# Kernel optimization log

Hardware: AMD Instinct MI355X
Metric: run time of the kernel (lower is better)

## Reference

```python
import jax, jax.numpy as jnp
import numpy as np

B, S, D, H, F = 4, 1024, 1024, 16, 4096
DK = D // H
NEG_INF = jnp.float32(-jnp.inf)


def rmsnorm(x, gamma):
    rms = jnp.sqrt(jnp.mean(x * x, axis=-1, keepdims=True))
    return gamma * x / rms


def masked_softmax(cor):
    # softmax over last dim; rows that are entirely -inf produce all-zero rows
    # (matches the original's NaN -> 0 masked_fill).
    m = jnp.max(cor, axis=-1, keepdims=True)
    m_safe = jnp.where(jnp.isneginf(m), 0.0, m)
    e = jnp.exp(cor - m_safe)
    denom = jnp.sum(e, axis=-1, keepdims=True)
    return e / jnp.where(denom == 0.0, 1.0, denom)


def setup_inputs() -> dict:
    key = jax.random.key(0)
    ks = jax.random.split(key, 12)
    inp = {
        'src': jax.random.normal(ks[0], (B, S, D), jnp.float32),
        'src_padding_mask': jax.random.bernoulli(ks[1], 0.1, (B, S)),
        'prev': jax.random.normal(ks[2], (H, B, S, S), jnp.float32),
        'layer_ind': 2,
        'Wq': jax.random.normal(ks[3], (H, D, DK), jnp.float32) * 0.02,
        'Wk': jax.random.normal(ks[4], (H, D, DK), jnp.float32) * 0.02,
        'Wv': jax.random.normal(ks[5], (H, D, DK), jnp.float32) * 0.02,
        'Wproj': jax.random.normal(ks[6], (D, D), jnp.float32) * 0.02,
        'gamma1': jnp.ones((D,), jnp.float32),
        'gamma2': jnp.ones((D,), jnp.float32),
        'W1': jax.random.normal(ks[7], (D, F), jnp.float32) * 0.02,
        'b1': jnp.zeros((F,), jnp.float32),
        'W2': jax.random.normal(ks[8], (F, D), jnp.float32) * 0.02,
        'b2': jnp.zeros((D,), jnp.float32),
    }
    return inp


def reference(src, src_padding_mask, prev, layer_ind, Wq, Wk, Wv, Wproj,
              gamma1, gamma2, W1, b1, W2, b2):
    ln1 = rmsnorm(src, gamma1)                              # [B,S,D]
    q = jnp.einsum('bsd,hdk->hbsk', ln1, Wq)                # [H,B,S,DK]
    k = jnp.einsum('bsd,hdk->hbsk', ln1, Wk)
    v = jnp.einsum('bsd,hdk->hbsk', ln1, Wv)
    scores = jnp.einsum('hbsk,hbtk->hbst', q, k) * (DK ** -0.5)  # [H,B,S,S]
    qmask = src_padding_mask[None, :, :, None]              # query (row) pad mask
    kvmask = src_padding_mask[None, :, None, :]             # key   (col) pad mask
    scores = jnp.where(qmask, NEG_INF, scores)
    scores = jnp.where(kvmask, NEG_INF, scores)
    raw = (scores + prev) / 2                               # RealFormer residual scores
    cor = raw / (1.0 - 0.5 ** layer_ind)
    w = masked_softmax(cor)                                 # [H,B,S,S]
    att = jnp.einsum('hbst,hbtk->bshk', w, v).reshape(B, S, H * DK)
    attention = att @ Wproj + src                           # residual
    h = jax.nn.relu(rmsnorm(attention, gamma2) @ W1 + b1)
    out = attention + (h @ W2 + b2)
    return out, raw
```

## Files before the change

kernel.cpp:

```cpp
#include <hip/hip_runtime.h>
#include <math.h>

#define Bv 4
#define Sv 1024
#define Dv 1024
#define Hv 16
#define Fv 4096
#define DKv 64

#define MASK_SENTINEL (-3.0e38f)

typedef __attribute__((ext_vector_type(8))) short short8v;
typedef __attribute__((ext_vector_type(4))) float float4v;

__device__ inline unsigned short bf16_rne(float x) {
    unsigned int u = __float_as_uint(x);
    unsigned int r = (u + 0x7FFFu + ((u >> 16) & 1u)) >> 16;
    return (unsigned short)r;
}
__device__ inline float bf16_tof(unsigned short h) {
    return __uint_as_float(((unsigned int)h) << 16);
}
__device__ inline void split2(float x, unsigned short& h, unsigned short& l) {
    unsigned short hh = bf16_rne(x);
    h = hh;
    l = bf16_rne(x - bf16_tof(hh));
}

__global__ __launch_bounds__(256) void rmsnorm_split_k(const float* __restrict__ x,
                                                       const float* __restrict__ g,
                                                       unsigned short* __restrict__ yh,
                                                       unsigned short* __restrict__ yl)
{
    const int row = blockIdx.x;
    const int tid = threadIdx.x;
    const float4* xv = reinterpret_cast<const float4*>(x) + (size_t)row * (Dv / 4);
    float4 v = xv[tid];
    float ss = v.x * v.x + v.y * v.y + v.z * v.z + v.w * v.w;
    #pragma unroll
    for (int o = 32; o > 0; o >>= 1) ss += __shfl_down(ss, o);
    __shared__ float wsum[4];
    if ((tid & 63) == 0) wsum[tid >> 6] = ss;
    __syncthreads();
    const float total = wsum[0] + wsum[1] + wsum[2] + wsum[3];
    const float rinv = rsqrtf(total * (1.0f / Dv));
    const float4 gv = reinterpret_cast<const float4*>(g)[tid];
    float o0 = v.x * gv.x * rinv, o1 = v.y * gv.y * rinv;
    float o2 = v.z * gv.z * rinv, o3 = v.w * gv.w * rinv;
    ushort4 uh, ul; unsigned short h, l;
    split2(o0, h, l); uh.x = h; ul.x = l;
    split2(o1, h, l); uh.y = h; ul.y = l;
    split2(o2, h, l); uh.z = h; ul.z = l;
    split2(o3, h, l); uh.w = h; ul.w = l;
    *(ushort4*)&yh[(size_t)row * Dv + tid * 4] = uh;
    *(ushort4*)&yl[(size_t)row * Dv + tid * 4] = ul;
}

template<bool HEADW>
__global__ __launch_bounds__(256) void tsplit_k(const float* __restrict__ W,
                                                unsigned short* __restrict__ WTh,
                                                unsigned short* __restrict__ WTl,
                                                int K, int N)
{
    __shared__ float tile[64 * 68];
    const int tid = threadIdx.x;
    const int n0 = blockIdx.x * 64, k0 = blockIdx.y * 64;
    #pragma unroll
    for (int it = 0; it < 4; ++it) {
        int slot = it * 256 + tid;
        int r = slot >> 4, c4 = (slot & 15) * 4;
        const float* src;
        if (HEADW)
            src = &W[((size_t)(n0 >> 6) * K + (k0 + r)) * 64 + c4];
        else
            src = &W[(size_t)(k0 + r) * N + n0 + c4];
        *(float4*)&tile[r * 68 + c4] = *(const float4*)src;
    }
    __syncthreads();
    #pragma unroll
    for (int it = 0; it < 4; ++it) {
        int slot = it * 256 + tid;
        int rr = slot >> 4, c4 = (slot & 15) * 4;
        ushort4 uh, ul;
        unsigned short h, l;
        split2(tile[(c4 + 0) * 68 + rr], h, l); uh.x = h; ul.x = l;
        split2(tile[(c4 + 1) * 68 + rr], h, l); uh.y = h; ul.y = l;
        split2(tile[(c4 + 2) * 68 + rr], h, l); uh.z = h; ul.z = l;
        split2(tile[(c4 + 3) * 68 + rr], h, l); uh.w = h; ul.w = l;
        size_t o = (size_t)(n0 + rr) * K + k0 + c4;
        *(ushort4*)&WTh[o] = uh;
        *(ushort4*)&WTl[o] = ul;
    }
}

#define BKP 40
#define KOFF ((size_t)8 << 20)
template<int OUTM, bool RELU, bool BIAS, bool RES>
__global__ __launch_bounds__(256) void gemm64(const unsigned short* __restrict__ Ahg,
                                              const unsigned short* __restrict__ Alg,
                                              const unsigned short* __restrict__ Bhg,
                                              const unsigned short* __restrict__ Blg,
                                              const float* __restrict__ bias,
                                              const float* __restrict__ res,
                                              float* __restrict__ C,
                                              unsigned short* __restrict__ Ch,
                                              unsigned short* __restrict__ Cl,
                                              int M, int N, int K)
{
    __shared__ unsigned short Ah[64 * BKP], Al[64 * BKP];
    __shared__ unsigned short Bh[128 * BKP], Bl[128 * BKP];
    const int tid = threadIdx.x;
    const int lane = tid & 63, wid = tid >> 6;
    const int wc = wid;
    const int l15 = lane & 15, lg = lane >> 4;
    const int bm = blockIdx.y * 64, bn = blockIdx.x * 128;

    float4v acc[4][2];
    #pragma unroll
    for (int i = 0; i < 4; ++i)
        #pragma unroll
        for (int j = 0; j < 2; ++j) acc[i][j] = (float4v)(0.0f);

    const int sr = tid >> 2, sc8 = (tid & 3) * 8;

    for (int k0 = 0; k0 < K; k0 += 32) {
        *(uint4*)&Ah[sr * BKP + sc8] = *(const uint4*)&Ahg[(size_t)(bm + sr) * K + k0 + sc8];
        *(uint4*)&Al[sr * BKP + sc8] = *(const uint4*)&Alg[(size_t)(bm + sr) * K + k0 + sc8];
        #pragma unroll
        for (int it = 0; it < 2; ++it) {
            int slot = it * 256 + tid;
            int r = slot >> 2, c8 = (slot & 3) * 8;
            *(uint4*)&Bh[r * BKP + c8] = *(const uint4*)&Bhg[(size_t)(bn + r) * K + k0 + c8];
            *(uint4*)&Bl[r * BKP + c8] = *(const uint4*)&Blg[(size_t)(bn + r) * K + k0 + c8];
        }
        __syncthreads();

        short8v fah[4], fal[4], fbh[2], fbl[2];
        const int kb = lg * 8;
        #pragma unroll
        for (int mi = 0; mi < 4; ++mi) {
            int row = mi * 16 + l15;
            fah[mi] = *(const short8v*)&Ah[row * BKP + kb];
            fal[mi] = *(const short8v*)&Al[row * BKP + kb];
        }
        #pragma unroll
        for (int ni = 0; ni < 2; ++ni) {
            int row = wc * 32 + ni * 16 + l15;
            fbh[ni] = *(const short8v*)&Bh[row * BKP + kb];
            fbl[ni] = *(const short8v*)&Bl[row * BKP + kb];
        }
        #pragma unroll
        for (int mi = 0; mi < 4; ++mi)
            #pragma unroll
            for (int ni = 0; ni < 2; ++ni) {
                float4v c = acc[mi][ni];
                c = __builtin_amdgcn_mfma_f32_16x16x32_bf16(fah[mi], fbh[ni], c, 0, 0, 0);
                c = __builtin_amdgcn_mfma_f32_16x16x32_bf16(fah[mi], fbl[ni], c, 0, 0, 0);
                c = __builtin_amdgcn_mfma_f32_16x16x32_bf16(fal[mi], fbh[ni], c, 0, 0, 0);
                acc[mi][ni] = c;
            }
        __syncthreads();
    }

    #pragma unroll
    for (int mi = 0; mi < 4; ++mi) {
        #pragma unroll
        for (int r = 0; r < 4; ++r) {
            int m = bm + mi * 16 + lg * 4 + r;
            #pragma unroll
            for (int ni = 0; ni < 2; ++ni) {
                int n = bn + wc * 32 + ni * 16 + l15;
                float v = acc[mi][ni][r];
                if (BIAS) v += bias[n];
                if (RELU) v = fmaxf(v, 0.0f);
                if (RES)  v += res[(size_t)m * N + n];
                if (OUTM == 0) {
                    C[(size_t)m * N + n] = v;
                } else if (OUTM == 1) {
                    unsigned short hi, lo;
                    split2(v, hi, lo);
                    Ch[(size_t)m * N + n] = hi;
                    Cl[(size_t)m * N + n] = lo;
                } else {
                    const int seg = n >> 10, nn = n & 1023;
                    if (seg == 2) {
                        C[(size_t)m * 1024 + nn] = v;
                    } else {
                        const int hh = nn >> 6, dk = nn & 63, bb = m >> 10, s = m & 1023;
                        size_t off = (((size_t)(hh * Bv + bb)) * Sv + s) * DKv + dk
                                   + (size_t)seg * KOFF;
                        unsigned short hi, lo;
                        split2(v, hi, lo);
                        Ch[off] = hi;
                        Cl[off] = lo;
                    }
                }
            }
        }
    }
}

__global__ __launch_bounds__(256) void scores_mfma_k(const unsigned short* __restrict__ qh,
                                                     const unsigned short* __restrict__ ql,
                                                     const unsigned short* __restrict__ kh,
                                                     const unsigned short* __restrict__ kl,
                                                     const float* __restrict__ prev,
                                                     const unsigned char* __restrict__ mask,
                                                     const int* __restrict__ layer_ind,
                                                     float* __restrict__ raw,
                                                     float2* __restrict__ stat2)
{
    __shared__ float T[4][16 * 68];
    const int tid = threadIdx.x;
    const int lane = tid & 63, wid = tid >> 6;
    const int wr = wid >> 1, wc = wid & 1;
    const int l15 = lane & 15, lg = lane >> 4;
    const int hb = blockIdx.y, b = hb & 3;
    const int sm = (blockIdx.x >> 3) * 64;
    const int tn = (blockIdx.x & 7) * 128;
    const float cs = 1.0f / (1.0f - exp2f(-(float)layer_ind[0]));

    float4v acc[2][4];
    #pragma unroll
    for (int i = 0; i < 2; ++i)
        #pragma unroll
        for (int j = 0; j < 4; ++j) acc[i][j] = (float4v)(0.0f);

    const size_t qbase = ((size_t)hb * Sv + sm + wr * 32) * DKv;
    const size_t kbase = ((size_t)hb * Sv + tn + wc * 64) * DKv;

    #pragma unroll
    for (int kk = 0; kk < 2; ++kk) {
        const int kb = kk * 32 + lg * 8;
        short8v fah[2], fal[2], fbh[4], fbl[4];
        #pragma unroll
        for (int mi = 0; mi < 2; ++mi) {
            size_t off = qbase + (size_t)(mi * 16 + l15) * DKv + kb;
            fah[mi] = *(const short8v*)&qh[off];
            fal[mi] = *(const short8v*)&ql[off];
        }
        #pragma unroll
        for (int ni = 0; ni < 4; ++ni) {
            size_t off = kbase + (size_t)(ni * 16 + l15) * DKv + kb;
            fbh[ni] = *(const short8v*)&kh[off];
            fbl[ni] = *(const short8v*)&kl[off];
        }
        #pragma unroll
        for (int mi = 0; mi < 2; ++mi)
            #pragma unroll
            for (int ni = 0; ni < 4; ++ni) {
                float4v c = acc[mi][ni];
                c = __builtin_amdgcn_mfma_f32_16x16x32_bf16(fah[mi], fbh[ni], c, 0, 0, 0);
                c = __builtin_amdgcn_mfma_f32_16x16x32_bf16(fah[mi], fbl[ni], c, 0, 0, 0);
                c = __builtin_amdgcn_mfma_f32_16x16x32_bf16(fal[mi], fbh[ni], c, 0, 0, 0);
                acc[mi][ni] = c;
            }
    }

    const int tb2 = (blockIdx.x & 7) * 2 + wc;

    #pragma unroll
    for (int mi = 0; mi < 2; ++mi) {
        #pragma unroll
        for (int ni = 0; ni < 4; ++ni)
            #pragma unroll
            for (int r = 0; r < 4; ++r)
                T[wid][(lg * 4 + r) * 68 + ni * 16 + l15] = acc[mi][ni][r];

        const int s = sm + wr * 32 + mi * 16 + l15;
        const bool qm = mask[b * Sv + s] != 0;
        float xv[16];
        #pragma unroll
        for (int c = 0; c < 4; ++c) {
            float4 tv = *(const float4*)&T[wid][l15 * 68 + lg * 16 + c * 4];
            const int t = tn + wc * 64 + lg * 16 + c * 4;
            const size_t off = ((size_t)hb * Sv + s) * Sv + t;
            const float4 pv = *(const float4*)&prev[off];
            const uchar4 km = *(const uchar4*)&mask[b * Sv + t];
            float4 o;
            o.x = (qm || km.x) ? MASK_SENTINEL : (tv.x * 0.125f + pv.x) * 0.5f;
            o.y = (qm || km.y) ? MASK_SENTINEL : (tv.y * 0.125f + pv.y) * 0.5f;
            o.z = (qm || km.z) ? MASK_SENTINEL : (tv.z * 0.125f + pv.z) * 0.5f;
            o.w = (qm || km.w) ? MASK_SENTINEL : (tv.w * 0.125f + pv.w) * 0.5f;
            *(float4*)&raw[off] = o;
            xv[c * 4 + 0] = (qm || km.x) ? -INFINITY : o.x * cs;
            xv[c * 4 + 1] = (qm || km.y) ? -INFINITY : o.y * cs;
            xv[c * 4 + 2] = (qm || km.z) ? -INFINITY : o.z * cs;
            xv[c * 4 + 3] = (qm || km.w) ? -INFINITY : o.w * cs;
        }

        float mx = -INFINITY;
        #pragma unroll
        for (int j = 0; j < 16; ++j) mx = fmaxf(mx, xv[j]);
        mx = fmaxf(mx, __shfl_xor(mx, 16));
        mx = fmaxf(mx, __shfl_xor(mx, 32));
        float se = 0.0f;
        #pragma unroll
        for (int j = 0; j < 16; ++j)
            se += (xv[j] == -INFINITY) ? 0.0f : __expf(xv[j] - mx);
        se += __shfl_xor(se, 16);
        se += __shfl_xor(se, 32);
        if (lg == 0) {
            float2 p; p.x = mx; p.y = se;
            stat2[(size_t)tb2 * (64 * Sv) + (size_t)hb * Sv + s] = p;
        }
    }
}

__global__ __launch_bounds__(256) void softmax_pv_k(const float* __restrict__ raw,
                                                    const float* __restrict__ v2d,
                                                    const float2* __restrict__ stat2,
                                                    const int* __restrict__ layer_ind,
                                                    unsigned short* __restrict__ att2dh,
                                                    unsigned short* __restrict__ att2dl)
{
    __shared__ float Vt[64 * 68];
    __shared__ float Wt[32 * 68];
    __shared__ float rowM[32], rowR[32];
    const int tid = threadIdx.x;
    const int hb = blockIdx.y, h = hb >> 2, b = hb & 3;
    const int s0 = blockIdx.x * 32;
    const float cs = 1.0f / (1.0f - exp2f(-(float)layer_ind[0]));

    if (tid < 32) {
        const size_t row = (size_t)hb * Sv + s0 + tid;
        float2 p[16];
        #pragma unroll
        for (int j = 0; j < 16; ++j) p[j] = stat2[(size_t)j * (64 * Sv) + row];
        float m = -INFINITY;
        #pragma unroll
        for (int j = 0; j < 16; ++j) m = fmaxf(m, p[j].x);
        float ssum = 0.0f;
        #pragma unroll
        for (int j = 0; j < 16; ++j)
            if (p[j].y > 0.0f) ssum += __expf(p[j].x - m) * p[j].y;
        rowM[tid] = (m == -INFINITY) ? 0.0f : m;
        rowR[tid] = (ssum == 0.0f) ? 1.0f : 1.0f / ssum;
    }
    __syncthreads();

    const int dk4 = (tid & 15) * 4;
    const int rp2 = tid >> 4;
    const int r0 = rp2 * 2, r1 = r0 + 1;
    float4 a0 = {0, 0, 0, 0}, a1 = {0, 0, 0, 0};

    const int wrow = tid >> 3, wc8 = (tid & 7) * 8;

    for (int tc = 0; tc < Sv; tc += 64) {
        #pragma unroll
        for (int it = 0; it < 4; ++it) {
            int slot = it * 256 + tid;
            int r = slot >> 4, c4 = (slot & 15) * 4;
            *(float4*)&Vt[r * 68 + c4] =
                *(const float4*)&v2d[((size_t)b * Sv + tc + r) * Dv + h * DKv + c4];
        }
        {
            const float mm = rowM[wrow], rc = rowR[wrow];
            const size_t off = ((size_t)hb * Sv + s0 + wrow) * Sv + tc + wc8;
            const float4 x0 = *(const float4*)&raw[off];
            const float4 x1 = *(const float4*)&raw[off + 4];
            float4 e0, e1;
            e0.x = (x0.x < -1e37f) ? 0.0f : __expf(x0.x * cs - mm) * rc;
            e0.y = (x0.y < -1e37f) ? 0.0f : __expf(x0.y * cs - mm) * rc;
            e0.z = (x0.z < -1e37f) ? 0.0f : __expf(x0.z * cs - mm) * rc;
            e0.w = (x0.w < -1e37f) ? 0.0f : __expf(x0.w * cs - mm) * rc;
            e1.x = (x1.x < -1e37f) ? 0.0f : __expf(x1.x * cs - mm) * rc;
            e1.y = (x1.y < -1e37f) ? 0.0f : __expf(x1.y * cs - mm) * rc;
            e1.z = (x1.z < -1e37f) ? 0.0f : __expf(x1.z * cs - mm) * rc;
            e1.w = (x1.w < -1e37f) ? 0.0f : __expf(x1.w * cs - mm) * rc;
            *(float4*)&Wt[wrow * 68 + wc8] = e0;
            *(float4*)&Wt[wrow * 68 + wc8 + 4] = e1;
        }
        __syncthreads();
        #pragma unroll 4
        for (int tt = 0; tt < 64; ++tt) {
            float4 vv = *(const float4*)&Vt[tt * 68 + dk4];
            float w0 = Wt[r0 * 68 + tt];
            float w1 = Wt[r1 * 68 + tt];
            a0.x = fmaf(w0, vv.x, a0.x); a0.y = fmaf(w0, vv.y, a0.y);
            a0.z = fmaf(w0, vv.z, a0.z); a0.w = fmaf(w0, vv.w, a0.w);
            a1.x = fmaf(w1, vv.x, a1.x); a1.y = fmaf(w1, vv.y, a1.y);
            a1.z = fmaf(w1, vv.z, a1.z); a1.w = fmaf(w1, vv.w, a1.w);
        }
        __syncthreads();
    }
    ushort4 uh, ul; unsigned short hh, ll;
    size_t o0 = ((size_t)b * Sv + s0 + r0) * Dv + h * DKv + dk4;
    size_t o1 = ((size_t)b * Sv + s0 + r1) * Dv + h * DKv + dk4;
    split2(a0.x, hh, ll); uh.x = hh; ul.x = ll;
    split2(a0.y, hh, ll); uh.y = hh; ul.y = ll;
    split2(a0.z, hh, ll); uh.z = hh; ul.z = ll;
    split2(a0.w, hh, ll); uh.w = hh; ul.w = ll;
    *(ushort4*)&att2dh[o0] = uh; *(ushort4*)&att2dl[o0] = ul;
    split2(a1.x, hh, ll); uh.x = hh; ul.x = ll;
    split2(a1.y, hh, ll); uh.y = hh; ul.y = ll;
    split2(a1.z, hh, ll); uh.z = hh; ul.z = ll;
    split2(a1.w, hh, ll); uh.w = hh; ul.w = ll;
    *(ushort4*)&att2dh[o1] = uh; *(ushort4*)&att2dl[o1] = ul;
}

extern "C" void kernel_launch(void* const* d_in, const int* in_sizes, int n_in,
                              void* d_out, int out_size, void* d_ws, size_t ws_size,
                              hipStream_t stream)
{
    const float* src          = (const float*)d_in[0];
    const unsigned char* mask = (const unsigned char*)d_in[1];
    const float* prev         = (const float*)d_in[2];
    const int* layer_ind      = (const int*)d_in[3];
    const float* Wq           = (const float*)d_in[4];
    const float* Wk           = (const float*)d_in[5];
    const float* Wv           = (const float*)d_in[6];
    const float* Wproj        = (const float*)d_in[7];
    const float* gamma1       = (const float*)d_in[8];
    const float* gamma2       = (const float*)d_in[9];
    const float* W1           = (const float*)d_in[10];
    const float* b1           = (const float*)d_in[11];
    const float* W2           = (const float*)d_in[12];
    const float* b2           = (const float*)d_in[13];

    float* out = (float*)d_out;
    float* raw = out + (size_t)Bv * Sv * Dv;

    float* ws = (float*)d_ws;
    unsigned short* S16 = (unsigned short*)d_ws;
    const size_t M1 = 1u << 20;
    unsigned short* WT1h = S16;
    unsigned short* WT1l = S16 + 4 * M1;
    unsigned short* WT2h = S16 + 8 * M1;
    unsigned short* WT2l = S16 + 12 * M1;
    unsigned short* WTallh = S16 + 16 * M1;
    unsigned short* WTalll = S16 + 19 * M1;
    unsigned short* WTph   = S16 + 22 * M1, *WTpl = S16 + 23 * M1;
    unsigned short* ln2h   = S16 + 16 * M1, *ln2l = S16 + 20 * M1;
    float* attn = ws + 12 * M1;
    unsigned short* ln1h = S16 + 32 * M1, *ln1l = S16 + 36 * M1;
    float2* stat2 = (float2*)(ws + 16 * M1);
    unsigned short* qh   = S16 + 40 * M1, *ql   = S16 + 44 * M1;
    unsigned short* kh   = S16 + 48 * M1, *kl   = S16 + 52 * M1;
    float* v2d = ws + 28 * M1;
    unsigned short* at2h = S16 + 40 * M1, *at2l = S16 + 44 * M1;
    unsigned short* hbufh = S16 + 32 * M1;
    unsigned short* hbufl = S16 + 48 * M1;
    (void)in_sizes; (void)n_in; (void)out_size; (void)ws_size;

    tsplit_k<true ><<<dim3(16, 16), 256, 0, stream>>>(Wq,    WTallh,          WTalll,          1024, 1024);
    tsplit_k<true ><<<dim3(16, 16), 256, 0, stream>>>(Wk,    WTallh + M1,     WTalll + M1,     1024, 1024);
    tsplit_k<true ><<<dim3(16, 16), 256, 0, stream>>>(Wv,    WTallh + 2 * M1, WTalll + 2 * M1, 1024, 1024);
    tsplit_k<false><<<dim3(16, 16), 256, 0, stream>>>(Wproj, WTph, WTpl, 1024, 1024);
    tsplit_k<false><<<dim3(64, 16), 256, 0, stream>>>(W1,    WT1h, WT1l, 1024, 4096);
    tsplit_k<false><<<dim3(16, 64), 256, 0, stream>>>(W2,    WT2h, WT2l, 4096, 1024);

    rmsnorm_split_k<<<4096, 256, 0, stream>>>(src, gamma1, ln1h, ln1l);

    gemm64<3, false, false, false><<<dim3(24, 64), 256, 0, stream>>>(ln1h, ln1l, WTallh, WTalll, nullptr, nullptr, v2d, qh, ql, 4096, 3072, 1024);

    scores_mfma_k<<<dim3(128, 64), 256, 0, stream>>>(qh, ql, kh, kl, prev, mask, layer_ind, raw, stat2);

    softmax_pv_k<<<dim3(32, 64), 256, 0, stream>>>(raw, v2d, stat2, layer_ind, at2h, at2l);

    gemm64<0, false, false, true><<<dim3(8, 64), 256, 0, stream>>>(at2h, at2l, WTph, WTpl, nullptr, src, attn, nullptr, nullptr, 4096, 1024, 1024);

    rmsnorm_split_k<<<4096, 256, 0, stream>>>(attn, gamma2, ln2h, ln2l);

    gemm64<1, true, true, false><<<dim3(32, 64), 256, 0, stream>>>(ln2h, ln2l, WT1h, WT1l, b1, nullptr, nullptr, hbufh, hbufl, 4096, 4096, 1024);

    gemm64<0, false, true, true><<<dim3(8, 64), 256, 0, stream>>>(hbufh, hbufl, WT2h, WT2l, b2, attn, out, nullptr, nullptr, 4096, 1024, 4096);
}
```

Before: 844.8 us.

## Fuse scores, online softmax and PV into one flash-style attention kernel

Replaces the separate scores kernel and the softmax-PV kernel with a single kernel that computes QK^T, writes raw, keeps a running max and sum per row, and accumulates P·V with split-bf16 MFMA. V is now written transposed in split bf16 by the QKV GEMM. prev tiles are streamed into LDS with swizzled global_load_lds so the next tile loads during the PV step. This removes the re-read of the 256MB raw tensor and the stat2 round trip, at the cost of more per-block serial work and fewer blocks (1024).

```diff
diff --git a/kernel.cpp b/kernel.cpp
--- a/kernel.cpp
+++ b/kernel.cpp
@@ -183,220 +183,214 @@
                     Cl[(size_t)m * N + n] = lo;
                 } else {
                     const int seg = n >> 10, nn = n & 1023;
-                    if (seg == 2) {
-                        C[(size_t)m * 1024 + nn] = v;
-                    } else {
-                        const int hh = nn >> 6, dk = nn & 63, bb = m >> 10, s = m & 1023;
-                        size_t off = (((size_t)(hh * Bv + bb)) * Sv + s) * DKv + dk
-                                   + (size_t)seg * KOFF;
-                        unsigned short hi, lo;
-                        split2(v, hi, lo);
-                        Ch[off] = hi;
-                        Cl[off] = lo;
-                    }
+                    const int hh = nn >> 6, dk = nn & 63, bb = m >> 10, s = m & 1023;
+                    unsigned short hi, lo;
+                    split2(v, hi, lo);
+                    size_t off;
+                    if (seg == 2)
+                        off = (((size_t)(hh * Bv + bb)) * DKv + dk) * Sv + s + 2 * KOFF;
+                    else
+                        off = (((size_t)(hh * Bv + bb)) * Sv + s) * DKv + dk
+                            + (size_t)seg * KOFF;
+                    Ch[off] = hi;
+                    Cl[off] = lo;
                 }
             }
         }
     }
 }
 
-__global__ __launch_bounds__(256) void scores_mfma_k(const unsigned short* __restrict__ qh,
-                                                     const unsigned short* __restrict__ ql,
-                                                     const unsigned short* __restrict__ kh,
-                                                     const unsigned short* __restrict__ kl,
-                                                     const float* __restrict__ prev,
-                                                     const unsigned char* __restrict__ mask,
-                                                     const int* __restrict__ layer_ind,
-                                                     float* __restrict__ raw,
-                                                     float2* __restrict__ stat2)
+__global__ __launch_bounds__(256) void attn_fused_k(const unsigned short* __restrict__ qh,
+                                                    const unsigned short* __restrict__ ql,
+                                                    const unsigned short* __restrict__ kh,
+                                                    const unsigned short* __restrict__ kl,
+                                                    const unsigned short* __restrict__ vth,
+                                                    const unsigned short* __restrict__ vtl,
+                                                    const float* __restrict__ prev,
+                                                    const unsigned char* __restrict__ mask,
+                                                    const int* __restrict__ layer_ind,
+                                                    float* __restrict__ raw,
+                                                    unsigned short* __restrict__ at2h,
+                                                    unsigned short* __restrict__ at2l)
 {
+    __shared__ float Pv[64 * 64];
     __shared__ float T[4][16 * 68];
+    __shared__ float SSc[4][16], SL[4][16];
     const int tid = threadIdx.x;
     const int lane = tid & 63, wid = tid >> 6;
-    const int wr = wid >> 1, wc = wid & 1;
     const int l15 = lane & 15, lg = lane >> 4;
-    const int hb = blockIdx.y, b = hb & 3;
-    const int sm = (blockIdx.x >> 3) * 64;
-    const int tn = (blockIdx.x & 7) * 128;
+    const int hb = blockIdx.y, b = hb & 3, h = hb >> 2;
+    const int sm = blockIdx.x * 64;
     const float cs = 1.0f / (1.0f - exp2f(-(float)layer_ind[0]));
-
-    float4v acc[2][4];
-    #pragma unroll
-    for (int i = 0; i < 2; ++i)
-        #pragma unroll
-        for (int j = 0; j < 4; ++j) acc[i][j] = (float4v)(0.0f);
-
-    const size_t qbase = ((size_t)hb * Sv + sm + wr * 32) * DKv;
-    const size_t kbase = ((size_t)hb * Sv + tn + wc * 64) * DKv;
-
-    #pragma unroll
-    for (int kk = 0; kk < 2; ++kk) {
-        const int kb = kk * 32 + lg * 8;
-        short8v fah[2], fal[2], fbh[4], fbl[4];
-        #pragma unroll
-        for (int mi = 0; mi < 2; ++mi) {
-            size_t off = qbase + (size_t)(mi * 16 + l15) * DKv + kb;
-            fah[mi] = *(const short8v*)&qh[off];
-            fal[mi] = *(const short8v*)&ql[off];
-        }
-        #pragma unroll
-        for (int ni = 0; ni < 4; ++ni) {
-            size_t off = kbase + (size_t)(ni * 16 + l15) * DKv + kb;
-            fbh[ni] = *(const short8v*)&kh[off];
-            fbl[ni] = *(const short8v*)&kl[off];
-        }
-        #pragma unroll
-        for (int mi = 0; mi < 2; ++mi)
-            #pragma unroll
-            for (int ni = 0; ni < 4; ++ni) {
-                float4v c = acc[mi][ni];
-                c = __builtin_amdgcn_mfma_f32_16x16x32_bf16(fah[mi], fbh[ni], c, 0, 0, 0);
-                c = __builtin_amdgcn_mfma_f32_16x16x32_bf16(fah[mi], fbl[ni], c, 0, 0, 0);
-                c = __builtin_amdgcn_mfma_f32_16x16x32_bf16(fal[mi], fbh[ni], c, 0, 0, 0);
-                acc[mi][ni] = c;
-            }
-    }
-
-    const int tb2 = (blockIdx.x & 7) * 2 + wc;
-
-    #pragma unroll
-    for (int mi = 0; mi < 2; ++mi) {
-        #pragma unroll
-        for (int ni = 0; ni < 4; ++ni)
+    const int srow = sm + wid * 16 + l15;
+    const bool qm = mask[b * Sv + srow] != 0;
+    const int rl = wid * 16 + l15;
+
+    short8v fqh[2], fql[2];
+    {
+        const size_t qb = ((size_t)hb * Sv + srow) * DKv + lg * 8;
+        fqh[0] = *(const short8v*)&qh[qb];
+        fqh[1] = *(const short8v*)&qh[qb + 32];
+        fql[0] = *(const short8v*)&ql[qb];
+        fql[1] = *(const short8v*)&ql[qb + 32];
+    }
+
+    float m_reg = -INFINITY, l_reg = 0.0f;
+    float4v apv[4];
+    #pragma unroll
+    for (int i = 0; i < 4; ++i) apv[i] = (float4v)(0.0f);
+
+    #pragma unroll
+    for (int it = 0; it < 4; ++it) {
+        const int gid = it * 256 + tid;
+        const int row = gid >> 4, gcol = gid & 15;
+        const int gs = gcol ^ (row & 7);
+        const float* gp = &prev[((size_t)hb * Sv + sm + row) * Sv + gs * 4];
+        __builtin_amdgcn_global_load_lds(
+            (const __attribute__((address_space(1))) void*)gp,
+            (__attribute__((address_space(3))) void*)&Pv[gid * 4], 16, 0, 0);
+    }
+
+    for (int kt = 0; kt < 16; ++kt) {
+        const int t0 = kt * 64;
+
+        float4v acc[4];
+        #pragma unroll
+        for (int i = 0; i < 4; ++i) acc[i] = (float4v)(0.0f);
+        #pragma unroll
+        for (int kk = 0; kk < 2; ++kk) {
+            #pragma unroll
+            for (int nf = 0; nf < 4; ++nf) {
+                const size_t off = ((size_t)hb * Sv + t0 + nf * 16 + l15) * DKv
+                                 + kk * 32 + lg * 8;
+                short8v fkh = *(const short8v*)&kh[off];
+                short8v fkl = *(const short8v*)&kl[off];
+                float4v c = acc[nf];
+                c = __builtin_amdgcn_mfma_f32_16x16x32_bf16(fqh[kk], fkh, c, 0, 0, 0);
+                c = __builtin_amdgcn_mfma_f32_16x16x32_bf16(fqh[kk], fkl, c, 0, 0, 0);
+                c = __builtin_amdgcn_mfma_f32_16x16x32_bf16(fql[kk], fkh, c, 0, 0, 0);
+                acc[nf] = c;
+            }
+        }
+
+        __syncthreads();
+
+        #pragma unroll
+        for (int nf = 0; nf < 4; ++nf)
             #pragma unroll
             for (int r = 0; r < 4; ++r)
-                T[wid][(lg * 4 + r) * 68 + ni * 16 + l15] = acc[mi][ni][r];
-
-        const int s = sm + wr * 32 + mi * 16 + l15;
-        const bool qm = mask[b * Sv + s] != 0;
+                T[wid][(lg * 4 + r) * 68 + nf * 16 + l15] = acc[nf][r];
+
         float xv[16];
         #pragma unroll
         for (int c = 0; c < 4; ++c) {
             float4 tv = *(const float4*)&T[wid][l15 * 68 + lg * 16 + c * 4];
-            const int t = tn + wc * 64 + lg * 16 + c * 4;
-            const size_t off = ((size_t)hb * Sv + s) * Sv + t;
-            const float4 pv = *(const float4*)&prev[off];
-            const uchar4 km = *(const uchar4*)&mask[b * Sv + t];
+            const int slot = (lg * 4 + c) ^ (rl & 7);
+            const float4 pv = *(const float4*)&Pv[rl * 64 + slot * 4];
+            const uchar4 km = *(const uchar4*)&mask[b * Sv + t0 + lg * 16 + c * 4];
             float4 o;
             o.x = (qm || km.x) ? MASK_SENTINEL : (tv.x * 0.125f + pv.x) * 0.5f;
             o.y = (qm || km.y) ? MASK_SENTINEL : (tv.y * 0.125f + pv.y) * 0.5f;
             o.z = (qm || km.z) ? MASK_SENTINEL : (tv.z * 0.125f + pv.z) * 0.5f;
             o.w = (qm || km.w) ? MASK_SENTINEL : (tv.w * 0.125f + pv.w) * 0.5f;
-            *(float4*)&raw[off] = o;
+            *(float4*)&raw[((size_t)hb * Sv + srow) * Sv + t0 + lg * 16 + c * 4] = o;
             xv[c * 4 + 0] = (qm || km.x) ? -INFINITY : o.x * cs;
             xv[c * 4 + 1] = (qm || km.y) ? -INFINITY : o.y * cs;
             xv[c * 4 + 2] = (qm || km.z) ? -INFINITY : o.z * cs;
             xv[c * 4 + 3] = (qm || km.w) ? -INFINITY : o.w * cs;
         }
 
-        float mx = -INFINITY;
-        #pragma unroll
-        for (int j = 0; j < 16; ++j) mx = fmaxf(mx, xv[j]);
-        mx = fmaxf(mx, __shfl_xor(mx, 16));
-        mx = fmaxf(mx, __shfl_xor(mx, 32));
-        float se = 0.0f;
-        #pragma unroll
-        for (int j = 0; j < 16; ++j)
-            se += (xv[j] == -INFINITY) ? 0.0f : __expf(xv[j] - mx);
-        se += __shfl_xor(se, 16);
-        se += __shfl_xor(se, 32);
-        if (lg == 0) {
-            float2 p; p.x = mx; p.y = se;
-            stat2[(size_t)tb2 * (64 * Sv) + (size_t)hb * Sv + s] = p;
-        }
-    }
-}
-
-__global__ __launch_bounds__(256) void softmax_pv_k(const float* __restrict__ raw,
-                                                    const float* __restrict__ v2d,
-                                                    const float2* __restrict__ stat2,
-                                                    const int* __restrict__ layer_ind,
-                                                    unsigned short* __restrict__ att2dh,
-                                                    unsigned short* __restrict__ att2dl)
-{
-    __shared__ float Vt[64 * 68];
-    __shared__ float Wt[32 * 68];
-    __shared__ float rowM[32], rowR[32];
-    const int tid = threadIdx.x;
-    const int hb = blockIdx.y, h = hb >> 2, b = hb & 3;
-    const int s0 = blockIdx.x * 32;
-    const float cs = 1.0f / (1.0f - exp2f(-(float)layer_ind[0]));
-
-    if (tid < 32) {
-        const size_t row = (size_t)hb * Sv + s0 + tid;
-        float2 p[16];
-        #pragma unroll
-        for (int j = 0; j < 16; ++j) p[j] = stat2[(size_t)j * (64 * Sv) + row];
-        float m = -INFINITY;
-        #pragma unroll
-        for (int j = 0; j < 16; ++j) m = fmaxf(m, p[j].x);
-        float ssum = 0.0f;
-        #pragma unroll
-        for (int j = 0; j < 16; ++j)
-            if (p[j].y > 0.0f) ssum += __expf(p[j].x - m) * p[j].y;
-        rowM[tid] = (m == -INFINITY) ? 0.0f : m;
-        rowR[tid] = (ssum == 0.0f) ? 1.0f : 1.0f / ssum;
-    }
-    __syncthreads();
-
-    const int dk4 = (tid & 15) * 4;
-    const int rp2 = tid >> 4;
-    const int r0 = rp2 * 2, r1 = r0 + 1;
-    float4 a0 = {0, 0, 0, 0}, a1 = {0, 0, 0, 0};
-
-    const int wrow = tid >> 3, wc8 = (tid & 7) * 8;
-
-    for (int tc = 0; tc < Sv; tc += 64) {
-        #pragma unroll
-        for (int it = 0; it < 4; ++it) {
-            int slot = it * 256 + tid;
-            int r = slot >> 4, c4 = (slot & 15) * 4;
-            *(float4*)&Vt[r * 68 + c4] =
-                *(const float4*)&v2d[((size_t)b * Sv + tc + r) * Dv + h * DKv + c4];
-        }
-        {
-            const float mm = rowM[wrow], rc = rowR[wrow];
-            const size_t off = ((size_t)hb * Sv + s0 + wrow) * Sv + tc + wc8;
-            const float4 x0 = *(const float4*)&raw[off];
-            const float4 x1 = *(const float4*)&raw[off + 4];
-            float4 e0, e1;
-            e0.x = (x0.x < -1e37f) ? 0.0f : __expf(x0.x * cs - mm) * rc;
-            e0.y = (x0.y < -1e37f) ? 0.0f : __expf(x0.y * cs - mm) * rc;
-            e0.z = (x0.z < -1e37f) ? 0.0f : __expf(x0.z * cs - mm) * rc;
-            e0.w = (x0.w < -1e37f) ? 0.0f : __expf(x0.w * cs - mm) * rc;
-            e1.x = (x1.x < -1e37f) ? 0.0f : __expf(x1.x * cs - mm) * rc;
-            e1.y = (x1.y < -1e37f) ? 0.0f : __expf(x1.y * cs - mm) * rc;
-            e1.z = (x1.z < -1e37f) ? 0.0f : __expf(x1.z * cs - mm) * rc;
-            e1.w = (x1.w < -1e37f) ? 0.0f : __expf(x1.w * cs - mm) * rc;
-            *(float4*)&Wt[wrow * 68 + wc8] = e0;
-            *(float4*)&Wt[wrow * 68 + wc8 + 4] = e1;
-        }
+        float tm = -INFINITY;
+        #pragma unroll
+        for (int j = 0; j < 16; ++j) tm = fmaxf(tm, xv[j]);
+        tm = fmaxf(tm, __shfl_xor(tm, 16));
+        tm = fmaxf(tm, __shfl_xor(tm, 32));
+        const float m_new = fmaxf(m_reg, tm);
+        float ts = 0.0f;
+        #pragma unroll
+        for (int j = 0; j < 16; ++j) {
+            const float e = (xv[j] == -INFINITY) ? 0.0f : __expf(xv[j] - m_new);
+            xv[j] = e;
+            ts += e;
+        }
+        ts += __shfl_xor(ts, 16);
+        ts += __shfl_xor(ts, 32);
+        const float scale = (m_reg == -INFINITY) ? 1.0f : __expf(m_reg - m_new);
+        l_reg = l_reg * scale + ts;
+        m_reg = m_new;
+        if (lg == 0) SSc[wid][l15] = scale;
+
+        #pragma unroll
+        for (int c = 0; c < 4; ++c) {
+            float4 e4;
+            e4.x = xv[c * 4 + 0]; e4.y = xv[c * 4 + 1];
+            e4.z = xv[c * 4 + 2]; e4.w = xv[c * 4 + 3];
+            *(float4*)&T[wid][l15 * 68 + lg * 16 + c * 4] = e4;
+        }
+
         __syncthreads();
-        #pragma unroll 4
-        for (int tt = 0; tt < 64; ++tt) {
-            float4 vv = *(const float4*)&Vt[tt * 68 + dk4];
-            float w0 = Wt[r0 * 68 + tt];
-            float w1 = Wt[r1 * 68 + tt];
-            a0.x = fmaf(w0, vv.x, a0.x); a0.y = fmaf(w0, vv.y, a0.y);
-            a0.z = fmaf(w0, vv.z, a0.z); a0.w = fmaf(w0, vv.w, a0.w);
-            a1.x = fmaf(w1, vv.x, a1.x); a1.y = fmaf(w1, vv.y, a1.y);
-            a1.z = fmaf(w1, vv.z, a1.z); a1.w = fmaf(w1, vv.w, a1.w);
-        }
-        __syncthreads();
-    }
-    ushort4 uh, ul; unsigned short hh, ll;
-    size_t o0 = ((size_t)b * Sv + s0 + r0) * Dv + h * DKv + dk4;
-    size_t o1 = ((size_t)b * Sv + s0 + r1) * Dv + h * DKv + dk4;
-    split2(a0.x, hh, ll); uh.x = hh; ul.x = ll;
-    split2(a0.y, hh, ll); uh.y = hh; ul.y = ll;
-    split2(a0.z, hh, ll); uh.z = hh; ul.z = ll;
-    split2(a0.w, hh, ll); uh.w = hh; ul.w = ll;
-    *(ushort4*)&att2dh[o0] = uh; *(ushort4*)&att2dl[o0] = ul;
-    split2(a1.x, hh, ll); uh.x = hh; ul.x = ll;
-    split2(a1.y, hh, ll); uh.y = hh; ul.y = ll;
-    split2(a1.z, hh, ll); uh.z = hh; ul.z = ll;
-    split2(a1.w, hh, ll); uh.w = hh; ul.w = ll;
-    *(ushort4*)&att2dh[o1] = uh; *(ushort4*)&att2dl[o1] = ul;
+
+        if (kt < 15) {
+            #pragma unroll
+            for (int it = 0; it < 4; ++it) {
+                const int gid = it * 256 + tid;
+                const int row = gid >> 4, gcol = gid & 15;
+                const int gs = gcol ^ (row & 7);
+                const float* gp = &prev[((size_t)hb * Sv + sm + row) * Sv + t0 + 64 + gs * 4];
+                __builtin_amdgcn_global_load_lds(
+                    (const __attribute__((address_space(1))) void*)gp,
+                    (__attribute__((address_space(3))) void*)&Pv[gid * 4], 16, 0, 0);
+            }
+        }
+
+        #pragma unroll
+        for (int r = 0; r < 4; ++r) {
+            const float sc = SSc[wid][lg * 4 + r];
+            #pragma unroll
+            for (int nf = 0; nf < 4; ++nf) apv[nf][r] *= sc;
+        }
+
+        #pragma unroll
+        for (int kc = 0; kc < 2; ++kc) {
+            short8v fa_h, fa_l;
+            #pragma unroll
+            for (int j = 0; j < 8; ++j) {
+                unsigned short hhv, llv;
+                split2(T[wid][l15 * 68 + kc * 32 + lg * 8 + j], hhv, llv);
+                fa_h[j] = (short)hhv;
+                fa_l[j] = (short)llv;
+            }
+            #pragma unroll
+            for (int nf = 0; nf < 4; ++nf) {
+                const size_t off = ((size_t)hb * DKv + nf * 16 + l15) * Sv
+                                 + t0 + kc * 32 + lg * 8;
+                short8v fvh = *(const short8v*)&vth[off];
+                short8v fvl = *(const short8v*)&vtl[off];
+                float4v c = apv[nf];
+                c = __builtin_amdgcn_mfma_f32_16x16x32_bf16(fa_h, fvh, c, 0, 0, 0);
+                c = __builtin_amdgcn_mfma_f32_16x16x32_bf16(fa_h, fvl, c, 0, 0, 0);
+                c = __builtin_amdgcn_mfma_f32_16x16x32_bf16(fa_l, fvh, c, 0, 0, 0);
+                apv[nf] = c;
+            }
+        }
+    }
+
+    if (lg == 0) SL[wid][l15] = l_reg;
+    #pragma unroll
+    for (int r = 0; r < 4; ++r) {
+        const float lr = SL[wid][lg * 4 + r];
+        const float rd = 1.0f / ((lr == 0.0f) ? 1.0f : lr);
+        const int s = sm + wid * 16 + lg * 4 + r;
+        #pragma unroll
+        for (int nf = 0; nf < 4; ++nf) {
+            const float v = apv[nf][r] * rd;
+            unsigned short hi, lo;
+            split2(v, hi, lo);
+            const size_t off = ((size_t)b * Sv + s) * Dv + h * DKv + nf * 16 + l15;
+            at2h[off] = hi;
+            at2l[off] = lo;
+        }
+    }
 }
 
 extern "C" void kernel_launch(void* const* d_in, const int* in_sizes, int n_in,
@@ -434,11 +428,10 @@
     unsigned short* ln2h   = S16 + 16 * M1, *ln2l = S16 + 20 * M1;
     float* attn = ws + 12 * M1;
     unsigned short* ln1h = S16 + 32 * M1, *ln1l = S16 + 36 * M1;
-    float2* stat2 = (float2*)(ws + 16 * M1);
     unsigned short* qh   = S16 + 40 * M1, *ql   = S16 + 44 * M1;
     unsigned short* kh   = S16 + 48 * M1, *kl   = S16 + 52 * M1;
-    float* v2d = ws + 28 * M1;
-    unsigned short* at2h = S16 + 40 * M1, *at2l = S16 + 44 * M1;
+    unsigned short* vth  = S16 + 56 * M1, *vtl  = S16 + 60 * M1;
+    unsigned short* at2h = S16 + 32 * M1, *at2l = S16 + 36 * M1;
     unsigned short* hbufh = S16 + 32 * M1;
     unsigned short* hbufl = S16 + 48 * M1;
     (void)in_sizes; (void)n_in; (void)out_size; (void)ws_size;
@@ -452,11 +445,9 @@
 
     rmsnorm_split_k<<<4096, 256, 0, stream>>>(src, gamma1, ln1h, ln1l);
 
-    gemm64<3, false, false, false><<<dim3(24, 64), 256, 0, stream>>>(ln1h, ln1l, WTallh, WTalll, nullptr, nullptr, v2d, qh, ql, 4096, 3072, 1024);
-
-    scores_mfma_k<<<dim3(128, 64), 256, 0, stream>>>(qh, ql, kh, kl, prev, mask, layer_ind, raw, stat2);
-
-    softmax_pv_k<<<dim3(32, 64), 256, 0, stream>>>(raw, v2d, stat2, layer_ind, at2h, at2l);
+    gemm64<3, false, false, false><<<dim3(24, 64), 256, 0, stream>>>(ln1h, ln1l, WTallh, WTalll, nullptr, nullptr, nullptr, qh, ql, 4096, 3072, 1024);
+
+    attn_fused_k<<<dim3(16, 64), 256, 0, stream>>>(qh, ql, kh, kl, vth, vtl, prev, mask, layer_ind, raw, at2h, at2l);
 
     gemm64<0, false, false, true><<<dim3(8, 64), 256, 0, stream>>>(at2h, at2l, WTph, WTpl, nullptr, src, attn, nullptr, nullptr, 4096, 1024, 1024);
 
```

Measured after the change: 859.2 us. Within noise of the previous version (+1.7%).
